# Optimization experiments

Measured on AMD Instinct MI355X. Metric: run time of the kernel, lower is better.

The kernel has to match this reference:

```python
import jax, jax.numpy as jnp
import numpy as np

N = 50000        # total nodes across batch
K = 16           # max neighbors per node (padded with index 0)
E = 800000       # directed edges / messages
B = 1024         # molecules
MAXM = 48        # max nodes per molecule (padded with index 0)
FEATURE_FDIM = 9
ALL_FDIM = 10    # feature_dist_graph (9) + reshaped rij distance (1)
H = 64           # hidden_dim
NUM_ITERS = 2
NEG_INF = -1e9


def setup_inputs() -> dict:
    key = jax.random.key(0)
    ks = jax.random.split(key, 16)
    s = 1.0 / np.sqrt(H)
    return {
        "target_features": jax.random.normal(ks[0], (N, FEATURE_FDIM), jnp.float32),
        "feature_dist_graph": jax.random.normal(ks[1], (E, ALL_FDIM - 1), jnp.float32),
        "rij_dist_pairs": jax.random.uniform(ks[2], (E,), jnp.float32),
        "start_end_env": jax.random.randint(ks[3], (N, K), 0, N + 1),
        "b_scope": jax.random.randint(ks[4], (N, K), 0, E),
        "l_scope": jax.random.randint(ks[5], (B, MAXM), 0, N + 1),
        "scope_update": jax.random.randint(ks[6], (E,), 0, N + 1),
        "scope_update_lig": jax.random.randint(ks[7], (E,), 0, N + 1),
        "W_emb": jax.random.uniform(ks[8], (FEATURE_FDIM, H), jnp.float32, 0.1, 0.9),
        "b_emb": jnp.zeros((H,), jnp.float32),
        "W_dist": jax.random.uniform(ks[9], (ALL_FDIM, H), jnp.float32, 0.1, 0.9),
        "b_dist": jnp.zeros((H,), jnp.float32),
        "W_gat": jax.random.normal(ks[10], (H, H), jnp.float32) * s,
        "Wm_gat": jax.random.normal(ks[11], (H, H), jnp.float32) * s,
        "a_gat": jax.random.normal(ks[12], (2 * H,), jnp.float32) * s,
    }


def reference(target_features, feature_dist_graph, rij_dist_pairs,
              start_end_env, b_scope, l_scope, scope_update, scope_update_lig,
              W_emb, b_emb, W_dist, b_dist, W_gat, Wm_gat, a_gat):
    # node embedding over origin features
    h = target_features @ W_emb + b_emb                        # [N, H]
    # edge message embedding over pair features + distance
    msg_in = jnp.concatenate([feature_dist_graph, rij_dist_pairs[:, None]], axis=1)
    message = msg_in @ W_dist + b_dist                         # [E, H]
    # prepend zero pad row (index 0 = padding for ragged gathers)
    hp = jnp.concatenate([jnp.zeros((1, H), h.dtype), h], axis=0)  # [N+1, H]
    pad_mask = (start_end_env == 0)                            # [N, K]
    upd_mask = (scope_update_lig > 0).astype(h.dtype)[:, None]  # [E, 1]
    for _ in range(NUM_ITERS):
        nb = hp[start_end_env]                                 # [N, K, H] gather neighbors
        mg = message[b_scope]                                  # [N, K, H] gather messages
        Wn = nb @ W_gat                                        # [N, K, H]
        Wm = mg @ Wm_gat                                       # [N, K, H]
        # GAT attention logits: leaky_relu(a^T [Wn || Wm])
        logits = jax.nn.leaky_relu(
            jnp.einsum('nkh,h->nk', Wn, a_gat[:H]) +
            jnp.einsum('nkh,h->nk', Wm, a_gat[H:]), 0.2)       # [N, K]
        logits = jnp.where(pad_mask, NEG_INF, logits)
        alpha = jax.nn.softmax(logits, axis=1)                 # [N, K]
        new_h = jax.nn.elu(jnp.einsum('nk,nkh->nh', alpha, Wn + Wm))  # [N, H]
        hp = jnp.concatenate([jnp.zeros((1, H), new_h.dtype), new_h], axis=0)
        # scatter updated node features back into edge messages
        message = hp[scope_update] * upd_mask                  # [E, H]
    cmp_enc = hp[l_scope]                                      # [B, MAXM, H]
    return cmp_enc.sum(axis=1)                                 # [B, H]
```

## Files before the change

kernel.cpp:

```cpp
#include <hip/hip_runtime.h>
#include <hip/hip_bf16.h>

#define N_NODES 50000
#define K_NB 16
#define E_EDGES 800000
#define B_MOL 1024
#define MAXM_M 48
#define FDIM 9
#define ADIM 10
#define H 64
#define NEG_INF_F (-1e9f)
#define PRE_NODE_BLOCKS 196
#define EDGE_BLOCKS 3125

__device__ inline float readlane_f(float v, int l) {
    return __int_as_float(__builtin_amdgcn_readlane(__float_as_int(v), l));
}
__device__ inline int readlane_i(int v, int l) {
    return __builtin_amdgcn_readlane(v, l);
}
__device__ inline float bf2f(unsigned u) {
    return __uint_as_float(u << 16);
}
__device__ inline unsigned short f2bf(float f) {
    unsigned x = __float_as_uint(f);
    return (unsigned short)((x + 0x7fffu + ((x >> 16) & 1u)) >> 16);
}

#define GLOAD_U16(dst, voff, sbase) \
    asm volatile("global_load_ushort %0, %1, %2" : "=v"(dst) : "v"(voff), "s"(sbase))
#define GLOAD_F32(dst, voff, sbase) \
    asm volatile("global_load_dword %0, %1, %2" : "=v"(dst) : "v"(voff), "s"(sbase))

#define DRAIN16(a) \
    asm volatile("s_waitcnt vmcnt(0)" \
        : "+v"(a[0]), "+v"(a[1]), "+v"(a[2]), "+v"(a[3]), \
          "+v"(a[4]), "+v"(a[5]), "+v"(a[6]), "+v"(a[7]), \
          "+v"(a[8]), "+v"(a[9]), "+v"(a[10]), "+v"(a[11]), \
          "+v"(a[12]), "+v"(a[13]), "+v"(a[14]), "+v"(a[15]))
#define HOLD16(a) \
    asm volatile("" \
        : "+v"(a[0]), "+v"(a[1]), "+v"(a[2]), "+v"(a[3]), \
          "+v"(a[4]), "+v"(a[5]), "+v"(a[6]), "+v"(a[7]), \
          "+v"(a[8]), "+v"(a[9]), "+v"(a[10]), "+v"(a[11]), \
          "+v"(a[12]), "+v"(a[13]), "+v"(a[14]), "+v"(a[15]))

__global__ __launch_bounds__(256) void k_fold(
    const float* __restrict__ W_emb, const float* __restrict__ b_emb,
    const float* __restrict__ W_dist, const float* __restrict__ b_dist,
    const float* __restrict__ W_gat, const float* __restrict__ Wm_gat,
    const float* __restrict__ a_gat,
    float* __restrict__ W2, float* __restrict__ c2,
    float* __restrict__ W3, float* __restrict__ c3,
    float* __restrict__ wa, float* __restrict__ ca,
    float* __restrict__ va, float* __restrict__ vb,
    float* __restrict__ wv9, float* __restrict__ cv)
{
    __shared__ float s_va[64], s_vb[64];
    int tid = threadIdx.x;
    int h = tid & 63, g = tid >> 6;
    if (g == 0) {
        float acc = 0.f;
        for (int t = 0; t < H; ++t) acc += W_gat[h * H + t] * a_gat[t];
        s_va[h] = acc; va[h] = acc;
    } else if (g == 1) {
        float acc = 0.f;
        for (int t = 0; t < H; ++t) acc += Wm_gat[h * H + t] * a_gat[H + t];
        s_vb[h] = acc; vb[h] = acc;
    } else if (g == 2) {
        float acc = 0.f;
        for (int t = 0; t < H; ++t) acc += b_dist[t] * Wm_gat[t * H + h];
        c2[h] = acc;
    } else {
        float acc = 0.f;
        for (int t = 0; t < H; ++t) acc += b_emb[t] * W_gat[t * H + h];
        c3[h] = acc;
    }
    __syncthreads();
    for (int q = tid; q < 640; q += 256) {
        int j = q >> 6, hh = q & 63;
        float acc = 0.f;
        for (int t = 0; t < H; ++t) acc += W_dist[j * H + t] * Wm_gat[t * H + hh];
        W2[q] = acc;
    }
    for (int q = tid; q < 576; q += 256) {
        int j = q >> 6, hh = q & 63;
        float acc = 0.f;
        for (int t = 0; t < H; ++t) acc += W_emb[j * H + t] * W_gat[t * H + hh];
        W3[q] = acc;
    }
    if (tid < ADIM) {
        float acc = 0.f;
        for (int t = 0; t < H; ++t) acc += W_dist[tid * H + t] * s_vb[t];
        wa[tid] = acc;
    } else if (tid == ADIM) {
        float acc = 0.f;
        for (int t = 0; t < H; ++t) acc += b_dist[t] * s_vb[t];
        ca[0] = acc;
    } else if (tid >= 16 && tid < 16 + FDIM) {
        int j = tid - 16;
        float acc = 0.f;
        for (int t = 0; t < H; ++t) acc += W_emb[j * H + t] * s_va[t];
        wv9[j] = acc;
    } else if (tid == 31) {
        float acc = 0.f;
        for (int t = 0; t < H; ++t) acc += b_emb[t] * s_va[t];
        cv[0] = acc;
    }
}

__global__ __launch_bounds__(256) void k_pre(
    const float* __restrict__ tf, const float* __restrict__ fdg,
    const float* __restrict__ rij,
    const int* __restrict__ su, const int* __restrict__ sul,
    const float* __restrict__ wa, const float* __restrict__ ca,
    const float* __restrict__ wv9, const float* __restrict__ cv,
    float* __restrict__ t1A, unsigned short* __restrict__ tfp,
    unsigned short* __restrict__ emsg, int* __restrict__ sue)
{
    int bid = blockIdx.x;
    if (bid < PRE_NODE_BLOCKS) {
        int n = bid * 256 + threadIdx.x;
        if (n == 0) {
            t1A[0] = 0.f;
            uint4 z = make_uint4(0, 0, 0, 0);
            ((uint4*)tfp)[0] = z; ((uint4*)tfp)[1] = z;
        }
        if (n >= N_NODES) return;
        float f[FDIM];
        float acc = cv[0];
#pragma unroll
        for (int j = 0; j < FDIM; ++j) {
            f[j] = tf[n * FDIM + j];
            acc += f[j] * wv9[j];
        }
        t1A[n + 1] = acc;
        unsigned rec[8];
#pragma unroll
        for (int j = 0; j < 4; ++j)
            rec[j] = (unsigned)f2bf(f[2 * j]) | ((unsigned)f2bf(f[2 * j + 1]) << 16);
        rec[4] = (unsigned)f2bf(f[8]);
        rec[5] = 0; rec[6] = 0; rec[7] = 0;
        uint4* dst = (uint4*)(tfp + (size_t)(n + 1) * 16);
        dst[0] = make_uint4(rec[0], rec[1], rec[2], rec[3]);
        dst[1] = make_uint4(rec[4], rec[5], rec[6], rec[7]);
    } else {
        int e = (bid - PRE_NODE_BLOCKS) * 256 + threadIdx.x;
        float f[ADIM];
#pragma unroll
        for (int j = 0; j < FDIM; ++j) f[j] = fdg[(size_t)e * FDIM + j];
        f[FDIM] = rij[e];
        float acc = ca[0];
#pragma unroll
        for (int j = 0; j < ADIM; ++j) acc += f[j] * wa[j];
        unsigned rec[8];
#pragma unroll
        for (int j = 0; j < 5; ++j)
            rec[j] = (unsigned)f2bf(f[2 * j]) | ((unsigned)f2bf(f[2 * j + 1]) << 16);
        rec[5] = __float_as_uint(acc);
        rec[6] = 0; rec[7] = 0;
        uint4* dst = (uint4*)(emsg + (size_t)e * 16);
        dst[0] = make_uint4(rec[0], rec[1], rec[2], rec[3]);
        dst[1] = make_uint4(rec[4], rec[5], rec[6], rec[7]);
        sue[e] = (sul[e] > 0) ? su[e] : 0;
    }
}

__global__ __launch_bounds__(256) void k_gat1(
    const int* __restrict__ sse, const int* __restrict__ bsc,
    const float* __restrict__ t1A, const unsigned short* __restrict__ tfp,
    const unsigned short* __restrict__ emsg,
    const float* __restrict__ W2, const float* __restrict__ c2,
    const float* __restrict__ W3, const float* __restrict__ c3,
    const float* __restrict__ va, const float* __restrict__ vb,
    unsigned short* __restrict__ hp2bf, float* __restrict__ t1B,
    float* __restrict__ t2B)
{
    int wave = threadIdx.x >> 6;
    int lane = threadIdx.x & 63;
    int n = blockIdx.x * 4 + wave;
    if (n == 0) {
        hp2bf[lane] = 0;
        if (lane == 0) { t1B[0] = 0.f; t2B[0] = 0.f; }
    }
    if (n >= N_NODES) return;

    int kidx = 0, ke = 0;
    float lg = NEG_INF_F;
    if (lane < K_NB) {
        kidx = sse[n * K_NB + lane];
        ke   = bsc[n * K_NB + lane];
        float g2 = __uint_as_float(*(const unsigned*)(emsg + (size_t)ke * 16 + 10));
        float p = t1A[kidx] + g2;
        p = (p > 0.f) ? p : 0.2f * p;
        lg = (kidx == 0) ? NEG_INF_F : p;
    }

    unsigned wn_u[K_NB], wm_u[K_NB];
    int offr = (lane & 15) * 2;
#pragma unroll
    for (int k = 0; k < K_NB; ++k) {
        const unsigned short* pk = tfp + (size_t)readlane_i(kidx, k) * 16;
        GLOAD_U16(wn_u[k], offr, pk);
    }
#pragma unroll
    for (int k = 0; k < K_NB; ++k) {
        const unsigned short* pe = emsg + (size_t)readlane_i(ke, k) * 16;
        GLOAD_U16(wm_u[k], offr, pe);
    }

    float m = lg;
#pragma unroll
    for (int o = 8; o > 0; o >>= 1) m = fmaxf(m, __shfl_xor(m, o, 64));
    float ex = __expf(lg - m);
    float s = ex;
#pragma unroll
    for (int o = 8; o > 0; o >>= 1) s += __shfl_xor(s, o, 64);
    float alpha = ex / s;

    DRAIN16(wn_u);
    HOLD16(wm_u);

    float fr = 0.f, frm = 0.f, beta = 0.f;
#pragma unroll
    for (int k = 0; k < K_NB; ++k) {
        float ak = readlane_f(alpha, k);
        fr  += ak * bf2f(wn_u[k]);
        frm += ak * bf2f(wm_u[k]);
        beta += (readlane_i(kidx, k) > 0) ? ak : 0.f;
    }
    float acc = c2[lane] + beta * c3[lane];
#pragma unroll
    for (int j = 0; j < FDIM; ++j) acc += readlane_f(fr, j) * W3[j * H + lane];
#pragma unroll
    for (int j = 0; j < ADIM; ++j) acc += readlane_f(frm, j) * W2[j * H + lane];
    float o = (acc > 0.f) ? acc : expm1f(acc);
    hp2bf[(size_t)(n + 1) * H + lane] = f2bf(o);
    float ta = o * va[lane], tb = o * vb[lane];
#pragma unroll
    for (int q = 32; q > 0; q >>= 1) {
        ta += __shfl_xor(ta, q, 64);
        tb += __shfl_xor(tb, q, 64);
    }
    if (lane == 0) { t1B[n + 1] = ta; t2B[n + 1] = tb; }
}

__global__ __launch_bounds__(256) void k_gat2(
    const int* __restrict__ sse, const int* __restrict__ bsc,
    const int* __restrict__ sue,
    const float* __restrict__ t1B, const float* __restrict__ t2B,
    const unsigned short* __restrict__ hp2bf,
    const float* __restrict__ W_gat, const float* __restrict__ Wm_gat,
    float* __restrict__ hp3)
{
    int wave = threadIdx.x >> 6;
    int lane = threadIdx.x & 63;
    int n = blockIdx.x * 4 + wave;
    if (n == 0) hp3[lane] = 0.f;
    if (n >= N_NODES) return;

    int kidx = 0, ksu = 0;
    float lg = NEG_INF_F;
    if (lane < K_NB) {
        kidx = sse[n * K_NB + lane];
        int ke = bsc[n * K_NB + lane];
        ksu = sue[ke];
        float p = t1B[kidx] + t2B[ksu];
        p = (p > 0.f) ? p : 0.2f * p;
        lg = (kidx == 0) ? NEG_INF_F : p;
    }

    unsigned wn_u[K_NB], wm_u[K_NB];
    int off = lane * 2;
#pragma unroll
    for (int k = 0; k < K_NB; ++k) {
        const unsigned short* pk = hp2bf + (size_t)readlane_i(kidx, k) * H;
        GLOAD_U16(wn_u[k], off, pk);
    }
#pragma unroll
    for (int k = 0; k < K_NB; ++k) {
        const unsigned short* ps = hp2bf + (size_t)readlane_i(ksu, k) * H;
        GLOAD_U16(wm_u[k], off, ps);
    }

    float m = lg;
#pragma unroll
    for (int o = 8; o > 0; o >>= 1) m = fmaxf(m, __shfl_xor(m, o, 64));
    float ex = __expf(lg - m);
    float s = ex;
#pragma unroll
    for (int o = 8; o > 0; o >>= 1) s += __shfl_xor(s, o, 64);
    float alpha = ex / s;

    DRAIN16(wn_u);
    HOLD16(wm_u);

    float gn = 0.f, gm = 0.f;
#pragma unroll
    for (int k = 0; k < K_NB; ++k) {
        float ak = readlane_f(alpha, k);
        gn += ak * bf2f(wn_u[k]);
        gm += ak * bf2f(wm_u[k]);
    }
    float acc = 0.f;
#pragma unroll
    for (int j = 0; j < H; ++j) {
        acc += readlane_f(gn, j) * W_gat[j * H + lane];
        acc += readlane_f(gm, j) * Wm_gat[j * H + lane];
    }
    float o = (acc > 0.f) ? acc : expm1f(acc);
    hp3[(size_t)(n + 1) * H + lane] = o;
}

__global__ __launch_bounds__(256) void k_out(
    const int* __restrict__ l_scope, const float* __restrict__ hp,
    float* __restrict__ out)
{
    int wave = threadIdx.x >> 6;
    int lane = threadIdx.x & 63;
    int b = blockIdx.x * 4 + wave;
    if (b >= B_MOL) return;
    int idx48 = (lane < MAXM_M) ? l_scope[b * MAXM_M + lane] : 0;
    float v[MAXM_M];
    int off = lane * 4;
#pragma unroll
    for (int m = 0; m < MAXM_M; ++m) {
        const float* pm = hp + (size_t)readlane_i(idx48, m) * H;
        GLOAD_F32(v[m], off, pm);
    }
    asm volatile("s_waitcnt vmcnt(0)"
        : "+v"(v[0]), "+v"(v[1]), "+v"(v[2]), "+v"(v[3]),
          "+v"(v[4]), "+v"(v[5]), "+v"(v[6]), "+v"(v[7]),
          "+v"(v[8]), "+v"(v[9]), "+v"(v[10]), "+v"(v[11]),
          "+v"(v[12]), "+v"(v[13]), "+v"(v[14]), "+v"(v[15]));
    asm volatile(""
        : "+v"(v[16]), "+v"(v[17]), "+v"(v[18]), "+v"(v[19]),
          "+v"(v[20]), "+v"(v[21]), "+v"(v[22]), "+v"(v[23]),
          "+v"(v[24]), "+v"(v[25]), "+v"(v[26]), "+v"(v[27]),
          "+v"(v[28]), "+v"(v[29]), "+v"(v[30]), "+v"(v[31]));
    asm volatile(""
        : "+v"(v[32]), "+v"(v[33]), "+v"(v[34]), "+v"(v[35]),
          "+v"(v[36]), "+v"(v[37]), "+v"(v[38]), "+v"(v[39]),
          "+v"(v[40]), "+v"(v[41]), "+v"(v[42]), "+v"(v[43]),
          "+v"(v[44]), "+v"(v[45]), "+v"(v[46]), "+v"(v[47]));
    float acc = 0.f;
#pragma unroll
    for (int m = 0; m < MAXM_M; ++m) acc += v[m];
    out[b * H + lane] = acc;
}

extern "C" void kernel_launch(void* const* d_in, const int* in_sizes, int n_in,
                              void* d_out, int out_size, void* d_ws, size_t ws_size,
                              hipStream_t stream)
{
    const float* tf     = (const float*)d_in[0];
    const float* fdg    = (const float*)d_in[1];
    const float* rij    = (const float*)d_in[2];
    const int*   sse    = (const int*)d_in[3];
    const int*   bsc    = (const int*)d_in[4];
    const int*   lsc    = (const int*)d_in[5];
    const int*   su     = (const int*)d_in[6];
    const int*   sul    = (const int*)d_in[7];
    const float* W_emb  = (const float*)d_in[8];
    const float* b_emb  = (const float*)d_in[9];
    const float* W_dist = (const float*)d_in[10];
    const float* b_dist = (const float*)d_in[11];
    const float* W_gat  = (const float*)d_in[12];
    const float* Wm_gat = (const float*)d_in[13];
    const float* a_gat  = (const float*)d_in[14];
    float* out = (float*)d_out;

    char* base = (char*)d_ws;
    size_t off = 0;
    auto alloc = [&](size_t bytes) {
        char* p = base + off;
        off = (off + bytes + 255) & ~(size_t)255;
        return p;
    };
    float* W2   = (float*)alloc(640 * 4);
    float* c2   = (float*)alloc(64 * 4);
    float* W3   = (float*)alloc(640 * 4);
    float* c3   = (float*)alloc(64 * 4);
    float* wa   = (float*)alloc(16 * 4);
    float* ca   = (float*)alloc(16 * 4);
    float* va   = (float*)alloc(64 * 4);
    float* vb   = (float*)alloc(64 * 4);
    float* wv9  = (float*)alloc(16 * 4);
    float* cv   = (float*)alloc(16 * 4);
    float* t1A  = (float*)alloc((size_t)(N_NODES + 1) * 4);
    float* t1B  = (float*)alloc((size_t)(N_NODES + 1) * 4);
    float* t2B  = (float*)alloc((size_t)(N_NODES + 1) * 4);
    int*   sue  = (int*)alloc((size_t)E_EDGES * 4);
    unsigned short* tfp   = (unsigned short*)alloc((size_t)(N_NODES + 1) * 16 * 2);
    unsigned short* hp2bf = (unsigned short*)alloc((size_t)(N_NODES + 1) * H * 2);
    char* big = alloc((size_t)E_EDGES * 32);
    unsigned short* emsg = (unsigned short*)big;
    float* hp3 = (float*)big;

    k_fold<<<dim3(1), dim3(256), 0, stream>>>(
        W_emb, b_emb, W_dist, b_dist, W_gat, Wm_gat, a_gat,
        W2, c2, W3, c3, wa, ca, va, vb, wv9, cv);

    k_pre<<<dim3(PRE_NODE_BLOCKS + EDGE_BLOCKS), dim3(256), 0, stream>>>(
        tf, fdg, rij, su, sul, wa, ca, wv9, cv, t1A, tfp, emsg, sue);

    dim3 gat_grid((N_NODES + 3) / 4);
    k_gat1<<<gat_grid, dim3(256), 0, stream>>>(
        sse, bsc, t1A, tfp, emsg, W2, c2, W3, c3, va, vb, hp2bf, t1B, t2B);

    k_gat2<<<gat_grid, dim3(256), 0, stream>>>(
        sse, bsc, sue, t1B, t2B, hp2bf, W_gat, Wm_gat, hp3);

    k_out<<<dim3(B_MOL / 4), dim3(256), 0, stream>>>(lsc, hp3, out);
}
```

Measured before the change: 233.0 us.

## Split second GAT projection into separate register-resident weight kernel

Moves the 64x128 weight projection out of the gather/softmax kernel into a new persistent-style kernel. There each lane keeps its column of W_gat and Wm_gat in registers and loops over rows, instead of reloading weights from global/cache for every node. The aggregated gn/gm vectors are packed as bf16 pairs into an intermediate buffer. This adds a kernel launch, an extra round trip of about 12.8MB of memory, and bf16 rounding of the aggregates before projection.

```diff
diff --git a/kernel.cpp b/kernel.cpp
--- a/kernel.cpp
+++ b/kernel.cpp
@@ -18,6 +18,9 @@
 }
 __device__ inline int readlane_i(int v, int l) {
     return __builtin_amdgcn_readlane(v, l);
+}
+__device__ inline unsigned readlane_u(unsigned v, int l) {
+    return (unsigned)__builtin_amdgcn_readlane((int)v, l);
 }
 __device__ inline float bf2f(unsigned u) {
     return __uint_as_float(u << 16);
@@ -250,13 +253,12 @@
     const int* __restrict__ sue,
     const float* __restrict__ t1B, const float* __restrict__ t2B,
     const unsigned short* __restrict__ hp2bf,
-    const float* __restrict__ W_gat, const float* __restrict__ Wm_gat,
-    float* __restrict__ hp3)
+    unsigned* __restrict__ gnm)
 {
     int wave = threadIdx.x >> 6;
     int lane = threadIdx.x & 63;
     int n = blockIdx.x * 4 + wave;
-    if (n == 0) hp3[lane] = 0.f;
+    if (n == 0) gnm[lane] = 0;
     if (n >= N_NODES) return;
 
     int kidx = 0, ksu = 0;
@@ -302,14 +304,35 @@
         gn += ak * bf2f(wn_u[k]);
         gm += ak * bf2f(wm_u[k]);
     }
-    float acc = 0.f;
+    gnm[(size_t)(n + 1) * H + lane] =
+        (unsigned)f2bf(gn) | ((unsigned)f2bf(gm) << 16);
+}
+
+__global__ __launch_bounds__(256) void k_proj(
+    const unsigned* __restrict__ gnm,
+    const float* __restrict__ W_gat, const float* __restrict__ Wm_gat,
+    float* __restrict__ hp3)
+{
+    int lane = threadIdx.x & 63;
+    float wg[H], wm[H];
 #pragma unroll
     for (int j = 0; j < H; ++j) {
-        acc += readlane_f(gn, j) * W_gat[j * H + lane];
-        acc += readlane_f(gm, j) * Wm_gat[j * H + lane];
-    }
-    float o = (acc > 0.f) ? acc : expm1f(acc);
-    hp3[(size_t)(n + 1) * H + lane] = o;
+        wg[j] = W_gat[j * H + lane];
+        wm[j] = Wm_gat[j * H + lane];
+    }
+    int row = blockIdx.x * 4 + (threadIdx.x >> 6);
+    int stride = gridDim.x * 4;
+    for (; row <= N_NODES; row += stride) {
+        unsigned u = gnm[(size_t)row * H + lane];
+        float acc = 0.f;
+#pragma unroll
+        for (int j = 0; j < H; ++j) {
+            unsigned uj = readlane_u(u, j);
+            acc += bf2f(uj & 0xffffu) * wg[j];
+            acc += bf2f(uj >> 16) * wm[j];
+        }
+        hp3[(size_t)row * H + lane] = (acc > 0.f) ? acc : expm1f(acc);
+    }
 }
 
 __global__ __launch_bounds__(256) void k_out(
@@ -393,6 +416,7 @@
     int*   sue  = (int*)alloc((size_t)E_EDGES * 4);
     unsigned short* tfp   = (unsigned short*)alloc((size_t)(N_NODES + 1) * 16 * 2);
     unsigned short* hp2bf = (unsigned short*)alloc((size_t)(N_NODES + 1) * H * 2);
+    unsigned* gnm = (unsigned*)alloc((size_t)(N_NODES + 1) * H * 4);
     char* big = alloc((size_t)E_EDGES * 32);
     unsigned short* emsg = (unsigned short*)big;
     float* hp3 = (float*)big;
@@ -409,7 +433,9 @@
         sse, bsc, t1A, tfp, emsg, W2, c2, W3, c3, va, vb, hp2bf, t1B, t2B);
 
     k_gat2<<<gat_grid, dim3(256), 0, stream>>>(
-        sse, bsc, sue, t1B, t2B, hp2bf, W_gat, Wm_gat, hp3);
+        sse, bsc, sue, t1B, t2B, hp2bf, gnm);
+
+    k_proj<<<dim3(1024), dim3(256), 0, stream>>>(gnm, W_gat, Wm_gat, hp3);
 
     k_out<<<dim3(B_MOL / 4), dim3(256), 0, stream>>>(lsc, hp3, out);
 }
```

Result: no change. 234.6 us (+0.7%).

## Use bf16 MFMA for the second GAT layer's projection via LDS tile

Applied to the files above, without the earlier changes.

The second GAT kernel now runs 16 nodes per 1024-thread block. Each wave computes its node's attention-weighted neighbour and message sums, packs them as bf16 into shared memory, and four waves run a 16x16x32 bf16 MFMA against an interleaved, pre-transposed bf16 copy of W_gat and Wm_gat built in k_fold. This replaces the per-lane 128-step readlane/FMA matrix-vector loop and its repeated weight loads. In exchange it adds a block-wide barrier, bf16 rounding of the aggregated vectors, and 1024-thread blocks that may lower occupancy flexibility.

```diff
diff --git a/kernel.cpp b/kernel.cpp
--- a/kernel.cpp
+++ b/kernel.cpp
@@ -12,6 +12,9 @@
 #define NEG_INF_F (-1e9f)
 #define PRE_NODE_BLOCKS 196
 #define EDGE_BLOCKS 3125
+
+typedef __bf16 bf16x8 __attribute__((ext_vector_type(8)));
+typedef float f32x4 __attribute__((ext_vector_type(4)));
 
 __device__ inline float readlane_f(float v, int l) {
     return __int_as_float(__builtin_amdgcn_readlane(__float_as_int(v), l));
@@ -54,7 +57,8 @@
     float* __restrict__ W3, float* __restrict__ c3,
     float* __restrict__ wa, float* __restrict__ ca,
     float* __restrict__ va, float* __restrict__ vb,
-    float* __restrict__ wv9, float* __restrict__ cv)
+    float* __restrict__ wv9, float* __restrict__ cv,
+    unsigned short* __restrict__ WintT)
 {
     __shared__ float s_va[64], s_vb[64];
     int tid = threadIdx.x;
@@ -88,6 +92,11 @@
         float acc = 0.f;
         for (int t = 0; t < H; ++t) acc += W_emb[j * H + t] * W_gat[t * H + hh];
         W3[q] = acc;
+    }
+    for (int q = tid; q < H * 2 * H; q += 256) {
+        int n = q >> 7, k = q & 127;
+        float v = (k & 1) ? Wm_gat[(k >> 1) * H + n] : W_gat[(k >> 1) * H + n];
+        WintT[q] = f2bf(v);
     }
     if (tid < ADIM) {
         float acc = 0.f;
@@ -245,71 +254,95 @@
     if (lane == 0) { t1B[n + 1] = ta; t2B[n + 1] = tb; }
 }
 
-__global__ __launch_bounds__(256) void k_gat2(
+__global__ __launch_bounds__(1024) void k_gat2(
     const int* __restrict__ sse, const int* __restrict__ bsc,
     const int* __restrict__ sue,
     const float* __restrict__ t1B, const float* __restrict__ t2B,
     const unsigned short* __restrict__ hp2bf,
-    const float* __restrict__ W_gat, const float* __restrict__ Wm_gat,
+    const unsigned short* __restrict__ WintT,
     float* __restrict__ hp3)
 {
+    __shared__ unsigned s_rows[16][72];
     int wave = threadIdx.x >> 6;
     int lane = threadIdx.x & 63;
-    int n = blockIdx.x * 4 + wave;
-    if (n == 0) hp3[lane] = 0.f;
-    if (n >= N_NODES) return;
-
-    int kidx = 0, ksu = 0;
-    float lg = NEG_INF_F;
-    if (lane < K_NB) {
-        kidx = sse[n * K_NB + lane];
-        int ke = bsc[n * K_NB + lane];
-        ksu = sue[ke];
-        float p = t1B[kidx] + t2B[ksu];
-        p = (p > 0.f) ? p : 0.2f * p;
-        lg = (kidx == 0) ? NEG_INF_F : p;
-    }
-
-    unsigned wn_u[K_NB], wm_u[K_NB];
-    int off = lane * 2;
-#pragma unroll
-    for (int k = 0; k < K_NB; ++k) {
-        const unsigned short* pk = hp2bf + (size_t)readlane_i(kidx, k) * H;
-        GLOAD_U16(wn_u[k], off, pk);
-    }
-#pragma unroll
-    for (int k = 0; k < K_NB; ++k) {
-        const unsigned short* ps = hp2bf + (size_t)readlane_i(ksu, k) * H;
-        GLOAD_U16(wm_u[k], off, ps);
-    }
-
-    float m = lg;
-#pragma unroll
-    for (int o = 8; o > 0; o >>= 1) m = fmaxf(m, __shfl_xor(m, o, 64));
-    float ex = __expf(lg - m);
-    float s = ex;
-#pragma unroll
-    for (int o = 8; o > 0; o >>= 1) s += __shfl_xor(s, o, 64);
-    float alpha = ex / s;
-
-    DRAIN16(wn_u);
-    HOLD16(wm_u);
+    int row  = blockIdx.x * 16 + wave;
+    int n    = row - 1;
 
     float gn = 0.f, gm = 0.f;
-#pragma unroll
-    for (int k = 0; k < K_NB; ++k) {
-        float ak = readlane_f(alpha, k);
-        gn += ak * bf2f(wn_u[k]);
-        gm += ak * bf2f(wm_u[k]);
-    }
-    float acc = 0.f;
-#pragma unroll
-    for (int j = 0; j < H; ++j) {
-        acc += readlane_f(gn, j) * W_gat[j * H + lane];
-        acc += readlane_f(gm, j) * Wm_gat[j * H + lane];
-    }
-    float o = (acc > 0.f) ? acc : expm1f(acc);
-    hp3[(size_t)(n + 1) * H + lane] = o;
+    if (n >= 0 && n < N_NODES) {
+        int kidx = 0, ksu = 0;
+        float lg = NEG_INF_F;
+        if (lane < K_NB) {
+            kidx = sse[n * K_NB + lane];
+            int ke = bsc[n * K_NB + lane];
+            ksu = sue[ke];
+            float p = t1B[kidx] + t2B[ksu];
+            p = (p > 0.f) ? p : 0.2f * p;
+            lg = (kidx == 0) ? NEG_INF_F : p;
+        }
+
+        unsigned wn_u[K_NB], wm_u[K_NB];
+        int off = lane * 2;
+#pragma unroll
+        for (int k = 0; k < K_NB; ++k) {
+            const unsigned short* pk = hp2bf + (size_t)readlane_i(kidx, k) * H;
+            GLOAD_U16(wn_u[k], off, pk);
+        }
+#pragma unroll
+        for (int k = 0; k < K_NB; ++k) {
+            const unsigned short* ps = hp2bf + (size_t)readlane_i(ksu, k) * H;
+            GLOAD_U16(wm_u[k], off, ps);
+        }
+
+        float m = lg;
+#pragma unroll
+        for (int o = 8; o > 0; o >>= 1) m = fmaxf(m, __shfl_xor(m, o, 64));
+        float ex = __expf(lg - m);
+        float s = ex;
+#pragma unroll
+        for (int o = 8; o > 0; o >>= 1) s += __shfl_xor(s, o, 64);
+        float alpha = ex / s;
+
+        DRAIN16(wn_u);
+        HOLD16(wm_u);
+
+#pragma unroll
+        for (int k = 0; k < K_NB; ++k) {
+            float ak = readlane_f(alpha, k);
+            gn += ak * bf2f(wn_u[k]);
+            gm += ak * bf2f(wm_u[k]);
+        }
+    }
+    s_rows[wave][lane] = (unsigned)f2bf(gn) | ((unsigned)f2bf(gm) << 16);
+    __syncthreads();
+
+    if (wave < 4) {
+        int t = wave;
+        int m = lane & 15, q = lane >> 4;
+        union UB { uint4 u; bf16x8 v; };
+        bf16x8 bfr[4];
+        const unsigned short* bp = WintT + (size_t)(t * 16 + m) * 128 + q * 8;
+#pragma unroll
+        for (int kk = 0; kk < 4; ++kk) {
+            UB ub; ub.u = *(const uint4*)(bp + kk * 32);
+            bfr[kk] = ub.v;
+        }
+        f32x4 acc = (f32x4){0.f, 0.f, 0.f, 0.f};
+#pragma unroll
+        for (int kk = 0; kk < 4; ++kk) {
+            UB ua; ua.u = *(const uint4*)&s_rows[m][kk * 16 + q * 4];
+            acc = __builtin_amdgcn_mfma_f32_16x16x32_bf16(ua.v, bfr[kk], acc, 0, 0, 0);
+        }
+        int row0 = blockIdx.x * 16;
+#pragma unroll
+        for (int r = 0; r < 4; ++r) {
+            int rr = row0 + q * 4 + r;
+            if (rr <= N_NODES) {
+                float v = acc[r];
+                hp3[(size_t)rr * H + t * 16 + m] = (v > 0.f) ? v : expm1f(v);
+            }
+        }
+    }
 }
 
 __global__ __launch_bounds__(256) void k_out(
@@ -387,6 +420,7 @@
     float* vb   = (float*)alloc(64 * 4);
     float* wv9  = (float*)alloc(16 * 4);
     float* cv   = (float*)alloc(16 * 4);
+    unsigned short* WintT = (unsigned short*)alloc(64 * 128 * 2);
     float* t1A  = (float*)alloc((size_t)(N_NODES + 1) * 4);
     float* t1B  = (float*)alloc((size_t)(N_NODES + 1) * 4);
     float* t2B  = (float*)alloc((size_t)(N_NODES + 1) * 4);
@@ -399,17 +433,16 @@
 
     k_fold<<<dim3(1), dim3(256), 0, stream>>>(
         W_emb, b_emb, W_dist, b_dist, W_gat, Wm_gat, a_gat,
-        W2, c2, W3, c3, wa, ca, va, vb, wv9, cv);
+        W2, c2, W3, c3, wa, ca, va, vb, wv9, cv, WintT);
 
     k_pre<<<dim3(PRE_NODE_BLOCKS + EDGE_BLOCKS), dim3(256), 0, stream>>>(
         tf, fdg, rij, su, sul, wa, ca, wv9, cv, t1A, tfp, emsg, sue);
 
-    dim3 gat_grid((N_NODES + 3) / 4);
-    k_gat1<<<gat_grid, dim3(256), 0, stream>>>(
+    k_gat1<<<dim3((N_NODES + 3) / 4), dim3(256), 0, stream>>>(
         sse, bsc, t1A, tfp, emsg, W2, c2, W3, c3, va, vb, hp2bf, t1B, t2B);
 
-    k_gat2<<<gat_grid, dim3(256), 0, stream>>>(
-        sse, bsc, sue, t1B, t2B, hp2bf, W_gat, Wm_gat, hp3);
+    k_gat2<<<dim3((N_NODES + 16) / 16), dim3(1024), 0, stream>>>(
+        sse, bsc, sue, t1B, t2B, hp2bf, WintT, hp3);
 
     k_out<<<dim3(B_MOL / 4), dim3(256), 0, stream>>>(lsc, hp3, out);
 }
```

New measurement: 208.4 us. 10.6% less time.
